# Kernel tuning notes

Measured on AMD Instinct MI355X. Metric: run time of the kernel, lower is better.

## Reference

```python
import jax, jax.numpy as jnp
import numpy as np

B, T, E, H, L, V = 16, 512, 512, 8, 4, 2048
HS = E // H  # head_size = n_embd // n_head
FF = 4 * E


def _ln(x, g, b):
    m = x.mean(-1, keepdims=True)
    v = ((x - m) ** 2).mean(-1, keepdims=True)
    return (x - m) * jax.lax.rsqrt(v + 1e-5) * g + b


def setup_inputs() -> dict:
    key = jax.random.key(0)
    ks = jax.random.split(key, 16)
    s = jnp.float32(0.02)
    return {
        "idx": jax.random.randint(ks[0], (B, T), 0, V),
        "tok_emb": jax.random.normal(ks[1], (V, E), jnp.float32) * s,
        "pos_emb": jax.random.normal(ks[2], (T, E), jnp.float32) * s,
        "Wq": jax.random.normal(ks[3], (L, E, E), jnp.float32) * s,
        "Wk": jax.random.normal(ks[4], (L, E, E), jnp.float32) * s,
        "Wv": jax.random.normal(ks[5], (L, E, E), jnp.float32) * s,
        "rel": jax.random.normal(ks[6], (L, 2 * T - 1, HS), jnp.float32) * s,
        "Wo": jax.random.normal(ks[7], (L, E, E), jnp.float32) * s,
        "bo": jnp.zeros((L, E), jnp.float32),
        "ln1_g": jnp.ones((L, E), jnp.float32),
        "ln1_b": jnp.zeros((L, E), jnp.float32),
        "W1": jax.random.normal(ks[8], (L, E, FF), jnp.float32) * s,
        "b1": jnp.zeros((L, FF), jnp.float32),
        "W2": jax.random.normal(ks[9], (L, FF, E), jnp.float32) * s,
        "b2": jnp.zeros((L, E), jnp.float32),
        "ln2_g": jnp.ones((L, E), jnp.float32),
        "ln2_b": jnp.zeros((L, E), jnp.float32),
        "lnf_g": jnp.ones((E,), jnp.float32),
        "lnf_b": jnp.zeros((E,), jnp.float32),
        "Wlm": jax.random.normal(ks[10], (E, V), jnp.float32) * s,
        "blm": jnp.zeros((V,), jnp.float32),
    }


def reference(idx, tok_emb, pos_emb, Wq, Wk, Wv, rel, Wo, bo, ln1_g, ln1_b,
              W1, b1, W2, b2, ln2_g, ln2_b, lnf_g, lnf_b, Wlm, blm):
    x = tok_emb[idx] + pos_emb[None, :T]  # (B,T,E)
    ri = jnp.arange(T)
    rel_idx = ri[:, None] - ri[None, :] + (T - 1)  # block_size == T
    causal = ri[:, None] >= ri[None, :]            # (T,T) lower-triangular
    scale = jnp.float32(1.0 / np.sqrt(HS))
    for l in range(L):
        h = _ln(x, ln1_g[l], ln1_b[l])
        # NOTE: torch code does .view(B, H, T, HS) on a (B, T, H*HS) tensor
        # (NOT a transpose) -- jnp.reshape matches row-major view semantics.
        q = (h @ Wq[l]).reshape(B, H, T, HS)
        k = (h @ Wk[l]).reshape(B, H, T, HS)
        v = (h @ Wv[l]).reshape(B, H, T, HS)
        re = rel[l][rel_idx]  # (T,T,HS)
        # rel scores: sum_d q[b,h,i,d]*re[i,j,d]; avoid the 5D intermediate
        scores = jnp.einsum('bhid,bhjd->bhij', q, k) * scale \
               + jnp.einsum('bhid,ijd->bhij', q, re)
        scores = jnp.where(causal, scores, -jnp.inf)
        att = jax.nn.softmax(scores, axis=-1)  # dropout disabled (eval)
        ctx = jnp.einsum('bhij,bhjd->bhid', att, v)
        ctx = jnp.swapaxes(ctx, 1, 2).reshape(B, T, H * HS)
        x = x + ctx @ Wo[l] + bo[l]
        h2 = _ln(x, ln2_g[l], ln2_b[l])
        x = x + jax.nn.relu(h2 @ W1[l] + b1[l]) @ W2[l] + b2[l]
    x = _ln(x, lnf_g, lnf_b)
    return x @ Wlm + blm  # logits (B,T,V)
```

## Files before the change

### kernel.cpp

```cpp
#include <hip/hip_runtime.h>
#include <hip/hip_bf16.h>
#include <stdint.h>

typedef __hip_bfloat16 bf16;
typedef __attribute__((ext_vector_type(8))) short bf16x8;
typedef __attribute__((ext_vector_type(8))) short short8;
typedef __attribute__((ext_vector_type(4))) float f32x4;

#define DEV __device__ __forceinline__

static constexpr int Bn = 16, Tn = 512, En = 512, Hn = 8, Ln = 4, Vn = 2048;
static constexpr int HSn = 64, FFn = 2048, Mn = Bn * Tn;
static constexpr int SQ = 1536;

DEV f32x4 mfma16(bf16x8 a, bf16x8 b, f32x4 c) {
  return __builtin_amdgcn_mfma_f32_16x16x32_bf16(a, b, c, 0, 0, 0);
}
DEV float b2f(bf16 x) { return __bfloat162float(x); }
DEV bf16 f2b(float x) { return __float2bfloat16(x); }

DEV void gload16(const void* g, void* l) {
  __builtin_amdgcn_global_load_lds(
      (const __attribute__((address_space(1))) void*)(uintptr_t)g,
      (__attribute__((address_space(3))) void*)(uint32_t)(uintptr_t)l, 16, 0, 0);
}

__global__ __launch_bounds__(256) void ktranspose(const float* __restrict__ in,
                                                  bf16* __restrict__ out, int R, int C,
                                                  long in_zs, long out_zs) {
  __shared__ float tile[32][33];
  int z = blockIdx.z;
  const float* inz = in + (size_t)z * in_zs;
  bf16* outz = out + (size_t)z * out_zs;
  int c0 = blockIdx.x * 32, r0 = blockIdx.y * 32;
  for (int k = 0; k < 32; k += 8)
    tile[threadIdx.y + k][threadIdx.x] =
        inz[(size_t)(r0 + threadIdx.y + k) * C + (c0 + threadIdx.x)];
  __syncthreads();
  for (int k = 0; k < 32; k += 8)
    outz[(size_t)(c0 + threadIdx.y + k) * R + (r0 + threadIdx.x)] =
        f2b(tile[threadIdx.x][threadIdx.y + k]);
}

__global__ __launch_bounds__(256) void kcast(const float* __restrict__ in,
                                             bf16* __restrict__ out, int n) {
  int i = blockIdx.x * 256 + threadIdx.x;
  if (i < n) out[i] = f2b(in[i]);
}

__global__ __launch_bounds__(256) void kembed(const int* __restrict__ idx,
                                              const float* __restrict__ tok,
                                              const float* __restrict__ pos,
                                              float* __restrict__ x) {
  int i = blockIdx.x * 256 + threadIdx.x;
  int e4 = (i & 127) * 4;
  int bt = i >> 7;
  int t = bt & (Tn - 1);
  f32x4 tv = *(const f32x4*)(tok + (size_t)idx[bt] * En + e4);
  f32x4 pv = *(const f32x4*)(pos + (size_t)t * En + e4);
  *(f32x4*)(x + (size_t)bt * En + e4) = tv + pv;
}

__global__ __launch_bounds__(256) void kln(const float* __restrict__ x,
                                           const float* __restrict__ g,
                                           const float* __restrict__ b,
                                           bf16* __restrict__ out) {
  int row = blockIdx.x * 4 + (threadIdx.x >> 6);
  int lane = threadIdx.x & 63;
  const float* xr = x + (size_t)row * En + lane * 8;
  f32x4 a0 = *(const f32x4*)xr;
  f32x4 a1 = *(const f32x4*)(xr + 4);
  float s = a0[0] + a0[1] + a0[2] + a0[3] + a1[0] + a1[1] + a1[2] + a1[3];
  for (int m = 1; m < 64; m <<= 1) s += __shfl_xor(s, m);
  float mean = s * (1.f / En);
  float s2 = 0.f;
  for (int j = 0; j < 4; j++) { float d0 = a0[j] - mean, d1 = a1[j] - mean; s2 += d0 * d0 + d1 * d1; }
  for (int m = 1; m < 64; m <<= 1) s2 += __shfl_xor(s2, m);
  float rstd = rsqrtf(s2 * (1.f / En) + 1e-5f);
  f32x4 g0 = *(const f32x4*)(g + lane * 8), g1 = *(const f32x4*)(g + lane * 8 + 4);
  f32x4 b0 = *(const f32x4*)(b + lane * 8), b1 = *(const f32x4*)(b + lane * 8 + 4);
  short8 ov;
  for (int j = 0; j < 4; j++) {
    bf16 h0 = f2b((a0[j] - mean) * rstd * g0[j] + b0[j]);
    bf16 h1 = f2b((a1[j] - mean) * rstd * g1[j] + b1[j]);
    ov[j] = reinterpret_cast<short&>(h0);
    ov[j + 4] = reinterpret_cast<short&>(h1);
  }
  *(short8*)(out + (size_t)row * En + lane * 8) = ov;
}

template <int BM, int BN, int DB, int SWZ, int NBIAS, int RELU, int MODE>
__global__ __launch_bounds__(256) void kgemm(const bf16* __restrict__ A,
                                             const bf16* __restrict__ Bt,
                                             const float* __restrict__ bias,
                                             float* __restrict__ outf,
                                             bf16* __restrict__ outh, int Ndim, int K) {
  constexpr int WM = BM / 2, WN = BN / 2, MI = WM / 16, NI = WN / 16;
  constexpr int NB = DB ? 2 : 1;
  __shared__ bf16 As[NB][BM * 64];
  __shared__ bf16 Bs[NB][BN * 64];
  int t = threadIdx.x, lane = t & 63, w = t >> 6;
  int lr = lane & 15, lg = lane >> 4;
  int sx = lr & 7;
  int wr = w >> 1, wc = w & 1;
  int bx, by;
  if (SWZ) {
    int id = blockIdx.x + gridDim.x * blockIdx.y;
    int xcd = id & 7, s = id >> 3;
    int gx = gridDim.x;
    by = xcd * 8 + s / gx;
    bx = s % gx;
  } else {
    bx = blockIdx.x; by = blockIdx.y;
  }
  int br = by * BM, bc = bx * BN;
  f32x4 acc[MI][NI] = {};
  int rl = lane >> 3, cb = (lane & 7) ^ rl;
  const bf16* Abase = A + (size_t)(br + w * (BM / 4) + rl) * K + cb * 8;
  const bf16* Bbase = Bt + (size_t)(bc + w * (BN / 4) + rl) * K + cb * 8;

  auto STAGE = [&](int buf, int kt) {
    for (int c = 0; c < BM / 32; c++)
      gload16(Abase + (size_t)(c * 8) * K + kt, &As[buf][(w * (BM / 4) + c * 8) * 64]);
    for (int c = 0; c < BN / 32; c++)
      gload16(Bbase + (size_t)(c * 8) * K + kt, &Bs[buf][(w * (BN / 4) + c * 8) * 64]);
  };
  auto COMPUTE = [&](int buf) {
    for (int kk = 0; kk < 2; kk++) {
      int gb = (kk * 4 + lg) ^ sx;
      bf16x8 af[MI], bfr[NI];
      for (int mi = 0; mi < MI; mi++)
        af[mi] = *(const bf16x8*)&As[buf][(wr * WM + mi * 16 + lr) * 64 + gb * 8];
      for (int ni = 0; ni < NI; ni++)
        bfr[ni] = *(const bf16x8*)&Bs[buf][(wc * WN + ni * 16 + lr) * 64 + gb * 8];
      for (int mi = 0; mi < MI; mi++)
        for (int ni = 0; ni < NI; ni++)
          acc[mi][ni] = mfma16(af[mi], bfr[ni], acc[mi][ni]);
    }
  };

  if (DB) {
    STAGE(0, 0);
    __syncthreads();
    int nt = K / 64;
    for (int t2 = 0; t2 < nt; t2++) {
      int cur = t2 & 1;
      if (t2 + 1 < nt) STAGE(cur ^ 1, (t2 + 1) * 64);
      COMPUTE(cur);
      __syncthreads();
    }
  } else {
    for (int kt = 0; kt < K; kt += 64) {
      __syncthreads();
      STAGE(0, kt);
      __syncthreads();
      COMPUTE(0);
    }
  }

  for (int mi = 0; mi < MI; mi++)
    for (int ni = 0; ni < NI; ni++)
      for (int r = 0; r < 4; r++) {
        int row = br + wr * WM + mi * 16 + lg * 4 + r;
        int col = bc + wc * WN + ni * 16 + lr;
        float val = acc[mi][ni][r];
        if (NBIAS) val += bias[col];
        if (RELU) val = fmaxf(val, 0.f);
        if (MODE == 1) outf[(size_t)row * Ndim + col] += val;
        else if (MODE == 2) outf[(size_t)row * Ndim + col] = val;
        else outh[(size_t)row * Ndim + col] = f2b(val);
      }
}

__global__ __launch_bounds__(256) void kattn(const bf16* __restrict__ qkv,
                                             const bf16* __restrict__ rel,
                                             bf16* __restrict__ ctx) {
  __shared__ bf16 Ks[64 * 64];
  __shared__ bf16 Vs[64 * 64];
  __shared__ bf16 Prel[4][16 * 81];
  __shared__ bf16 Ps[4][16 * 64];
  int pairp = blockIdx.x, bh = blockIdx.y;
  int b = bh >> 3, hh = bh & 7;
  int t = threadIdx.x, lane = t & 63, w = t >> 6;
  int lr = lane & 15, lg = lane >> 4;
  int sx = lr & 7;
  int rl8 = lane >> 3, cbk = (lane & 7) ^ rl8;
  const size_t headrow = (size_t)(b * Tn + hh * 64);
  bf16* prw = &Prel[w][0];
  bf16* psw = &Ps[w][0];
  int jp = t >> 3, db = (t & 7) * 8;

  for (int ph = 0; ph < 2; ph++) {
    int iblk = ph ? (7 - pairp) : pairp;
    int i0w = iblk * 64 + w * 16;
    bf16x8 aq[2];
    {
      int t2 = i0w + lr;
      const bf16* qp = qkv + (headrow + (t2 >> 3)) * SQ + (t2 & 7) * 64;
      aq[0] = *(const bf16x8*)(qp + lg * 8);
      aq[1] = *(const bf16x8*)(qp + 32 + lg * 8);
    }
    f32x4 o[4] = {};
    float m_run = -3e38f, l_run = 0.f;

    for (int jb = 0; jb <= iblk * 64; jb += 64) {
      bool diag = (jb == iblk * 64);
      int j0 = jb + jp * 2;
      bf16x8 va = *(const bf16x8*)(qkv + (headrow + (j0 >> 3)) * SQ + (j0 & 7) * 64 + 1024 + db);
      bf16x8 vb2 = *(const bf16x8*)(qkv + (headrow + ((j0 + 1) >> 3)) * SQ + ((j0 + 1) & 7) * 64 + 1024 + db);
      __syncthreads();
      for (int c = 0; c < 2; c++) {
        int row = w * 16 + c * 8 + rl8;
        const bf16* src = qkv + (headrow + ((jb + row) >> 3)) * SQ +
                          (row & 7) * 64 + 512 + cbk * 8;
        gload16(src, &Ks[(w * 16 + c * 8) * 64]);
      }
      {
        const short* pa = (const short*)&va;
        const short* pb = (const short*)&vb2;
        for (int u = 0; u < 8; u++) {
          int d = db + u;
          int idx = d * 64 + (((jp >> 2) ^ (d & 7)) * 8) + (jp & 3) * 2;
          uint32_t pk = (uint32_t)(uint16_t)pa[u] | ((uint32_t)(uint16_t)pb[u] << 16);
          *(uint32_t*)((short*)Vs + idx) = pk;
        }
      }
      __syncthreads();
      int njmax = diag ? w : 3;
      int nmmin = diag ? 3 - w : 0;
      __builtin_amdgcn_s_setprio(1);
      f32x4 sqk[4] = {};
      for (int nj = 0; nj <= njmax; nj++) {
        int row = nj * 16 + lr;
        bf16x8 kb0 = *(const bf16x8*)&Ks[row * 64 + ((lg ^ sx) * 8)];
        bf16x8 kb1 = *(const bf16x8*)&Ks[row * 64 + (((4 + lg) ^ sx) * 8)];
        sqk[nj] = mfma16(kb0, aq[0], sqk[nj]);
        sqk[nj] = mfma16(kb1, aq[1], sqk[nj]);
      }
      int base = i0w - jb + 448;
      for (int nm = nmmin; nm < 5; nm++) {
        int mrow = base + nm * 16 + lr;
        if (mrow > 1022) mrow = 1022;
        const bf16* rp = rel + (size_t)mrow * 64;
        f32x4 sr = {};
        sr = mfma16(aq[0], *(const bf16x8*)(rp + lg * 8), sr);
        sr = mfma16(aq[1], *(const bf16x8*)(rp + 32 + lg * 8), sr);
        for (int r = 0; r < 4; r++)
          prw[(lg * 4 + r) * 81 + nm * 16 + lr] = f2b(sr[r]);
      }
      __builtin_amdgcn_s_setprio(0);
      float sv[4][4];
      for (int nj = 0; nj < 4; nj++)
        for (int r = 0; r < 4; r++) sv[nj][r] = -3e38f;
      float mloc = -3e38f;
      for (int nj = 0; nj <= njmax; nj++)
        for (int r = 0; r < 4; r++) {
          int jj = nj * 16 + lg * 4 + r;
          float val = sqk[nj][r] * 0.125f + b2f(prw[lr * 81 + (lr - jj + 63)]);
          if (jb + jj > i0w + lr) val = -3e38f;
          sv[nj][r] = val;
          mloc = fmaxf(mloc, val);
        }
      mloc = fmaxf(mloc, __shfl_xor(mloc, 16));
      mloc = fmaxf(mloc, __shfl_xor(mloc, 32));
      float mnew = fmaxf(m_run, mloc);
      float corr = __expf(m_run - mnew);
      m_run = mnew;
      float lsum = 0.f;
      for (int nj = 0; nj < 4; nj++)
        for (int r = 0; r < 4; r++) {
          float p = __expf(sv[nj][r] - mnew);
          lsum += p;
          psw[lr * 64 + (((nj * 2 + (lg >> 1)) ^ sx) * 8) + (lg & 1) * 4 + r] = f2b(p);
        }
      lsum += __shfl_xor(lsum, 16);
      lsum += __shfl_xor(lsum, 32);
      l_run = l_run * corr + lsum;
      for (int r = 0; r < 4; r++) {
        float c = __shfl(corr, lg * 4 + r);
        for (int nd = 0; nd < 4; nd++) o[nd][r] *= c;
      }
      __builtin_amdgcn_s_setprio(1);
      bf16x8 ap0 = *(const bf16x8*)&psw[lr * 64 + ((lg ^ sx) * 8)];
      bf16x8 ap1 = *(const bf16x8*)&psw[lr * 64 + (((4 + lg) ^ sx) * 8)];
      for (int nd = 0; nd < 4; nd++) {
        int d = nd * 16 + lr;
        bf16x8 vb0 = *(const bf16x8*)&Vs[d * 64 + ((lg ^ sx) * 8)];
        bf16x8 vb1 = *(const bf16x8*)&Vs[d * 64 + (((4 + lg) ^ sx) * 8)];
        o[nd] = mfma16(ap0, vb0, o[nd]);
        o[nd] = mfma16(ap1, vb1, o[nd]);
      }
      __builtin_amdgcn_s_setprio(0);
    }
    for (int r = 0; r < 4; r++) {
      float linv = 1.f / __shfl(l_run, lg * 4 + r);
      int row = i0w + lg * 4 + r;
      for (int nd = 0; nd < 4; nd++)
        ctx[((size_t)b * Tn + row) * En + hh * 64 + nd * 16 + lr] = f2b(o[nd][r] * linv);
    }
  }
}

extern "C" void kernel_launch(void* const* d_in, const int* in_sizes, int n_in,
                              void* d_out, int out_size, void* d_ws, size_t ws_size,
                              hipStream_t stream) {
  (void)in_sizes; (void)n_in; (void)out_size; (void)ws_size;
  const int* idx = (const int*)d_in[0];
  const float* tok = (const float*)d_in[1];
  const float* pos = (const float*)d_in[2];
  const float* Wq = (const float*)d_in[3];
  const float* Wk = (const float*)d_in[4];
  const float* Wv = (const float*)d_in[5];
  const float* rel = (const float*)d_in[6];
  const float* Wo = (const float*)d_in[7];
  const float* bo = (const float*)d_in[8];
  const float* ln1_g = (const float*)d_in[9];
  const float* ln1_b = (const float*)d_in[10];
  const float* W1 = (const float*)d_in[11];
  const float* b1 = (const float*)d_in[12];
  const float* W2 = (const float*)d_in[13];
  const float* b2 = (const float*)d_in[14];
  const float* ln2_g = (const float*)d_in[15];
  const float* ln2_b = (const float*)d_in[16];
  const float* lnf_g = (const float*)d_in[17];
  const float* lnf_b = (const float*)d_in[18];
  const float* Wlm = (const float*)d_in[19];
  const float* blm = (const float*)d_in[20];

  char* ws = (char*)d_ws;
  float* x = (float*)(ws + 0);
  bf16* h = (bf16*)(ws + 16777216);
  bf16* qkv = (bf16*)(ws + 25165824);
  bf16* ctx = (bf16*)(ws + 50331648);
  bf16* ffn1 = qkv;
  bf16* wqkvT = (bf16*)(ws + 58720256);
  bf16* woT = wqkvT + (size_t)Ln * SQ * En;
  bf16* w1T = woT + (size_t)Ln * En * En;
  bf16* w2T = w1T + (size_t)Ln * En * FFn;
  bf16* wlmT = w2T + (size_t)Ln * FFn * En;
  bf16* relc = wlmT + (size_t)En * Vn;
  float* outf = (float*)d_out;

  dim3 tb(32, 8);
  ktranspose<<<dim3(16, 16, Ln), tb, 0, stream>>>(Wq, wqkvT, En, En, (long)En * En, (long)SQ * En);
  ktranspose<<<dim3(16, 16, Ln), tb, 0, stream>>>(Wk, wqkvT + 512 * 512, En, En, (long)En * En, (long)SQ * En);
  ktranspose<<<dim3(16, 16, Ln), tb, 0, stream>>>(Wv, wqkvT + 2 * 512 * 512, En, En, (long)En * En, (long)SQ * En);
  ktranspose<<<dim3(16, 16, Ln), tb, 0, stream>>>(Wo, woT, En, En, (long)En * En, (long)En * En);
  ktranspose<<<dim3(64, 16, Ln), tb, 0, stream>>>(W1, w1T, En, FFn, (long)En * FFn, (long)En * FFn);
  ktranspose<<<dim3(16, 64, Ln), tb, 0, stream>>>(W2, w2T, FFn, En, (long)FFn * En, (long)FFn * En);
  ktranspose<<<dim3(64, 16, 1), tb, 0, stream>>>(Wlm, wlmT, En, Vn, 0, 0);
  kcast<<<(Ln * (2 * Tn - 1) * HSn + 255) / 256, 256, 0, stream>>>(
      rel, relc, Ln * (2 * Tn - 1) * HSn);

  kembed<<<(Mn * En / 4) / 256, 256, 0, stream>>>(idx, tok, pos, x);

  for (int l = 0; l < Ln; l++) {
    kln<<<Mn / 4, 256, 0, stream>>>(x, ln1_g + (size_t)l * En, ln1_b + (size_t)l * En, h);
    kgemm<128, 128, 0, 1, 0, 0, 0><<<dim3(12, 64), 256, 0, stream>>>(
        h, wqkvT + (size_t)l * SQ * En, nullptr, nullptr, qkv, SQ, En);
    kattn<<<dim3(4, 128), 256, 0, stream>>>(
        qkv, relc + (size_t)l * (2 * Tn - 1) * HSn, ctx);
    kgemm<128, 128, 1, 1, 1, 0, 1><<<dim3(4, 64), 256, 0, stream>>>(
        ctx, woT + (size_t)l * En * En, bo + (size_t)l * En, x, nullptr, En, En);
    kln<<<Mn / 4, 256, 0, stream>>>(x, ln2_g + (size_t)l * En, ln2_b + (size_t)l * En, h);
    kgemm<128, 128, 0, 1, 1, 1, 0><<<dim3(16, 64), 256, 0, stream>>>(
        h, w1T + (size_t)l * En * FFn, b1 + (size_t)l * FFn, nullptr, ffn1, FFn, En);
    kgemm<128, 128, 1, 1, 1, 0, 1><<<dim3(4, 64), 256, 0, stream>>>(
        ffn1, w2T + (size_t)l * FFn * En, b2 + (size_t)l * En, x, nullptr, En, FFn);
  }
  kln<<<Mn / 4, 256, 0, stream>>>(x, lnf_g, lnf_b, h);
  kgemm<128, 128, 0, 1, 1, 0, 2><<<dim3(16, 64), 256, 0, stream>>>(
      h, wlmT, blm, outf, nullptr, Vn, En);
}
```

Measured before the change: 709.9 us.

## Split attention key range across two blocks and merge partials in a combine kernel

The attention grid doubles so that each (batch, head, query pair) is handled by two blocks. Each block processes alternating 64-key tiles and writes an unnormalized bf16 partial output plus its per-row running max and sum. A new kcombine kernel rescales and merges the two partials into ctx. Block ids are also remapped so that heads spread across XCDs. The aim is more parallelism and occupancy for attention, at the cost of an extra kernel launch, extra global traffic for the partials, and some precision loss from storing unnormalized partials in bf16.

```diff
diff --git a/kernel.cpp b/kernel.cpp
--- a/kernel.cpp
+++ b/kernel.cpp
@@ -18,6 +18,8 @@
 }
 DEV float b2f(bf16 x) { return __bfloat162float(x); }
 DEV bf16 f2b(float x) { return __float2bfloat16(x); }
+DEV short f2s(float x) { bf16 h = f2b(x); return reinterpret_cast<short&>(h); }
+DEV float s2f(short x) { return __bfloat162float(reinterpret_cast<bf16&>(x)); }
 
 DEV void gload16(const void* g, void* l) {
   __builtin_amdgcn_global_load_lds(
@@ -81,10 +83,8 @@
   f32x4 b0 = *(const f32x4*)(b + lane * 8), b1 = *(const f32x4*)(b + lane * 8 + 4);
   short8 ov;
   for (int j = 0; j < 4; j++) {
-    bf16 h0 = f2b((a0[j] - mean) * rstd * g0[j] + b0[j]);
-    bf16 h1 = f2b((a1[j] - mean) * rstd * g1[j] + b1[j]);
-    ov[j] = reinterpret_cast<short&>(h0);
-    ov[j + 4] = reinterpret_cast<short&>(h1);
+    ov[j] = f2s((a0[j] - mean) * rstd * g0[j] + b0[j]);
+    ov[j + 4] = f2s((a1[j] - mean) * rstd * g1[j] + b1[j]);
   }
   *(short8*)(out + (size_t)row * En + lane * 8) = ov;
 }
@@ -174,12 +174,18 @@
 
 __global__ __launch_bounds__(256) void kattn(const bf16* __restrict__ qkv,
                                              const bf16* __restrict__ rel,
-                                             bf16* __restrict__ ctx) {
+                                             bf16* __restrict__ part0,
+                                             bf16* __restrict__ part1,
+                                             float2* __restrict__ ml) {
   __shared__ bf16 Ks[64 * 64];
   __shared__ bf16 Vs[64 * 64];
   __shared__ bf16 Prel[4][16 * 81];
   __shared__ bf16 Ps[4][16 * 64];
-  int pairp = blockIdx.x, bh = blockIdx.y;
+  int rawid = blockIdx.x + 8 * blockIdx.y;
+  int xcd = rawid & 7, s = rawid >> 3;
+  int bh = xcd + 8 * (s & 15);
+  int rest = s >> 4;
+  int pairp = rest >> 1, jhalf = rest & 1;
   int b = bh >> 3, hh = bh & 7;
   int t = threadIdx.x, lane = t & 63, w = t >> 6;
   int lr = lane & 15, lg = lane >> 4;
@@ -188,6 +194,7 @@
   const size_t headrow = (size_t)(b * Tn + hh * 64);
   bf16* prw = &Prel[w][0];
   bf16* psw = &Ps[w][0];
+  bf16* pbuf = jhalf ? part1 : part0;
   int jp = t >> 3, db = (t & 7) * 8;
 
   for (int ph = 0; ph < 2; ph++) {
@@ -203,7 +210,7 @@
     f32x4 o[4] = {};
     float m_run = -3e38f, l_run = 0.f;
 
-    for (int jb = 0; jb <= iblk * 64; jb += 64) {
+    for (int jb = jhalf * 64; jb <= iblk * 64; jb += 128) {
       bool diag = (jb == iblk * 64);
       int j0 = jb + jp * 2;
       bf16x8 va = *(const bf16x8*)(qkv + (headrow + (j0 >> 3)) * SQ + (j0 & 7) * 64 + 1024 + db);
@@ -293,12 +300,36 @@
       __builtin_amdgcn_s_setprio(0);
     }
     for (int r = 0; r < 4; r++) {
-      float linv = 1.f / __shfl(l_run, lg * 4 + r);
       int row = i0w + lg * 4 + r;
       for (int nd = 0; nd < 4; nd++)
-        ctx[((size_t)b * Tn + row) * En + hh * 64 + nd * 16 + lr] = f2b(o[nd][r] * linv);
-    }
+        pbuf[((size_t)b * Tn + row) * En + hh * 64 + nd * 16 + lr] = f2b(o[nd][r]);
+    }
+    if (lane < 16)
+      ml[(size_t)jhalf * 65536 + (size_t)bh * Tn + i0w + lr] = make_float2(m_run, l_run);
   }
+}
+
+__global__ __launch_bounds__(256) void kcombine(bf16* __restrict__ p0,
+                                                const bf16* __restrict__ p1,
+                                                const float2* __restrict__ ml) {
+  int tid = blockIdx.x * 256 + threadIdx.x;
+  int dchunk = tid & 7;
+  int q = tid >> 3;
+  int hh = q & 7, g = q >> 3;
+  int i = g & (Tn - 1), b = g >> 9;
+  int bh = b * 8 + hh;
+  float2 m1 = ml[(size_t)bh * Tn + i];
+  float2 m2 = ml[65536 + (size_t)bh * Tn + i];
+  float mx = fmaxf(m1.x, m2.x);
+  float a1 = __expf(m1.x - mx), a2 = __expf(m2.x - mx);
+  float linv = 1.f / (m1.y * a1 + m2.y * a2);
+  size_t base = (size_t)g * En + hh * 64 + dchunk * 8;
+  short8 o1 = *(const short8*)(p0 + base);
+  short8 o2 = *(const short8*)(p1 + base);
+  short8 ov;
+  for (int u = 0; u < 8; u++)
+    ov[u] = f2s((s2f(o1[u]) * a1 + s2f(o2[u]) * a2) * linv);
+  *(short8*)(p0 + base) = ov;
 }
 
 extern "C" void kernel_launch(void* const* d_in, const int* in_sizes, int n_in,
@@ -339,6 +370,7 @@
   bf16* w2T = w1T + (size_t)Ln * En * FFn;
   bf16* wlmT = w2T + (size_t)Ln * FFn * En;
   bf16* relc = wlmT + (size_t)En * Vn;
+  float2* mlbuf = (float2*)(ws + 87031808);
   float* outf = (float*)d_out;
 
   dim3 tb(32, 8);
@@ -358,8 +390,9 @@
     kln<<<Mn / 4, 256, 0, stream>>>(x, ln1_g + (size_t)l * En, ln1_b + (size_t)l * En, h);
     kgemm<128, 128, 0, 1, 0, 0, 0><<<dim3(12, 64), 256, 0, stream>>>(
         h, wqkvT + (size_t)l * SQ * En, nullptr, nullptr, qkv, SQ, En);
-    kattn<<<dim3(4, 128), 256, 0, stream>>>(
-        qkv, relc + (size_t)l * (2 * Tn - 1) * HSn, ctx);
+    kattn<<<dim3(8, 128), 256, 0, stream>>>(
+        qkv, relc + (size_t)l * (2 * Tn - 1) * HSn, ctx, h, mlbuf);
+    kcombine<<<2048, 256, 0, stream>>>(ctx, h, mlbuf);
     kgemm<128, 128, 1, 1, 1, 0, 1><<<dim3(4, 64), 256, 0, stream>>>(
         ctx, woT + (size_t)l * En * En, bo + (size_t)l * En, x, nullptr, En, En);
     kln<<<Mn / 4, 256, 0, stream>>>(x, ln2_g + (size_t)l * En, ln2_b + (size_t)l * En, h);
```

Measured after the change: 735.9 us. +3.7%, slower.
